# Kernel optimization log

Measured on AMD Instinct MI355X. Metric: run time of the kernel, lower is better.

## Reference

```python
import jax, jax.numpy as jnp
import numpy as np

H = 16
QK_NOPE = 128
QK_ROPE = 64
QK_HEAD = 192
V_HEAD = 128
KV_LORA = 512
Q_LORA = 1536
HIDDEN = 2048
ROPE_THETA = 500000.0
EPS = 1e-6


def _rms_norm(x, w, eps=EPS):
    var = jnp.mean(x * x, axis=-1, keepdims=True)
    return w * (x * jax.lax.rsqrt(var + eps))


def _rotate_half(x):
    d = x.shape[-1] // 2
    return jnp.concatenate([-x[..., d:], x[..., :d]], axis=-1)


def _rope_cos_sin(T, dim, theta, dtype):
    inv_freq = 1.0 / (theta ** (jnp.arange(0, dim, 2, dtype=jnp.float32) / dim))
    t = jnp.arange(T, dtype=jnp.float32)
    freqs = jnp.outer(t, inv_freq)               # [T, dim//2]
    emb = jnp.concatenate([freqs, freqs], axis=-1)  # [T, dim]
    return jnp.cos(emb).astype(dtype), jnp.sin(emb).astype(dtype)


def _apply_rope_interleave(q, k, cos, sin):
    # deinterleave: [x0,x1,x2,...] -> [x0,x2,... , x1,x3,...]
    def deint(x):
        return jnp.concatenate([x[..., 0::2], x[..., 1::2]], axis=-1)
    q, k = deint(q), deint(k)
    cos = cos[None, None]  # [1,1,T,d]
    sin = sin[None, None]
    q_e = q * cos + _rotate_half(q) * sin
    k_e = k * cos + _rotate_half(k) * sin
    return q_e, k_e


def setup_inputs() -> dict:
    key = jax.random.key(0)
    ks = jax.random.split(key, 8)
    s = 0.02
    B, T = 2, 2048
    return {
        "x": jax.random.normal(ks[0], (B, T, HIDDEN), jnp.float32),
        "q_a_w": jax.random.normal(ks[1], (HIDDEN, Q_LORA), jnp.float32) * s,
        "q_a_ln_w": jnp.ones((Q_LORA,), jnp.float32),
        "q_b_w": jax.random.normal(ks[2], (Q_LORA, H * QK_HEAD), jnp.float32) * s,
        "kv_a_w": jax.random.normal(ks[3], (HIDDEN, KV_LORA + QK_ROPE), jnp.float32) * s,
        "kv_a_ln_w": jnp.ones((KV_LORA,), jnp.float32),
        "kv_b_w": jax.random.normal(ks[4], (KV_LORA, H * (QK_NOPE + V_HEAD)), jnp.float32) * s,
        "o_w": jax.random.normal(ks[5], (H * V_HEAD, HIDDEN), jnp.float32) * s,
    }


def reference(x, q_a_w, q_a_ln_w, q_b_w, kv_a_w, kv_a_ln_w, kv_b_w, o_w):
    B, T, _ = x.shape
    scale = QK_HEAD ** -0.5

    # Q path: hidden -> q_lora -> RMSNorm -> H*qk_head
    q = _rms_norm(x @ q_a_w, q_a_ln_w) @ q_b_w
    q = q.reshape(B, T, H, QK_HEAD).transpose(0, 2, 1, 3)  # [B,H,T,qk_head]
    q_nope, q_rope = q[..., :QK_NOPE], q[..., QK_NOPE:]

    # KV path: hidden -> kv_lora + rope_dim
    ckv = x @ kv_a_w
    kv_c, k_rope = ckv[..., :KV_LORA], ckv[..., KV_LORA:]
    kv = _rms_norm(kv_c, kv_a_ln_w) @ kv_b_w
    kv = kv.reshape(B, T, H, QK_NOPE + V_HEAD).transpose(0, 2, 1, 3)
    k_nope, v = kv[..., :QK_NOPE], kv[..., QK_NOPE:]

    k_rope = k_rope.reshape(B, 1, T, QK_ROPE)
    cos, sin = _rope_cos_sin(T, QK_ROPE, ROPE_THETA, x.dtype)
    q_rope, k_rope = _apply_rope_interleave(q_rope, k_rope, cos, sin)
    k_rope = jnp.broadcast_to(k_rope, (B, H, T, QK_ROPE))

    qf = jnp.concatenate([q_nope, q_rope], axis=-1)  # [B,H,T,192]
    kf = jnp.concatenate([k_nope, k_rope], axis=-1)

    # causal SDPA
    scores = jnp.einsum("bhqd,bhkd->bhqk", qf, kf) * scale
    causal = jnp.tril(jnp.ones((T, T), bool))
    scores = jnp.where(causal[None, None], scores, jnp.finfo(scores.dtype).min)
    attn = jax.nn.softmax(scores, axis=-1)
    out = jnp.einsum("bhqk,bhkd->bhqd", attn, v)  # [B,H,T,128]
    out = out.transpose(0, 2, 1, 3).reshape(B, T, H * V_HEAD)
    return out @ o_w
```

## Files before the change

### kernel.cpp

```cpp
#include <hip/hip_runtime.h>
#include <hip/hip_bf16.h>
#include <cstdint>


typedef __bf16 bf16;
typedef __bf16 bf16x8 __attribute__((ext_vector_type(8)));
typedef __bf16 bf16x4v __attribute__((ext_vector_type(4)));
typedef float f32x4 __attribute__((ext_vector_type(4)));

#define TSEQ 2048
#define MR 4096

typedef const uint32_t __attribute__((address_space(1))) * gas1_t;
typedef uint32_t __attribute__((address_space(3))) * las3_t;

static __device__ __forceinline__ void gload_lds16(const void* g, void* l) {
  __builtin_amdgcn_global_load_lds(
      reinterpret_cast<gas1_t>(reinterpret_cast<uintptr_t>(g)),
      reinterpret_cast<las3_t>(reinterpret_cast<uintptr_t>(l)), 16, 0, 0);
}

static __device__ __forceinline__ f32x4 mfma16(bf16x8 a, bf16x8 b, f32x4 c) {
  return __builtin_amdgcn_mfma_f32_16x16x32_bf16(a, b, c, 0, 0, 0);
}


__global__ __launch_bounds__(256) void k_cvt_bf16(const float* __restrict__ in,
                                                  bf16* __restrict__ out) {
  int i = blockIdx.x * 256 + threadIdx.x;
  float4 f = reinterpret_cast<const float4*>(in)[i];
  bf16x4v o = {(bf16)f.x, (bf16)f.y, (bf16)f.z, (bf16)f.w};
  reinterpret_cast<bf16x4v*>(out)[i] = o;
}

__global__ __launch_bounds__(256) void k_zerofill(bf16* __restrict__ p) {
  uint4 z = make_uint4(0, 0, 0, 0);
  reinterpret_cast<uint4*>(p)[blockIdx.x * 256 + threadIdx.x] = z;
}

__global__ __launch_bounds__(256) void k_transpose(const float* __restrict__ W,
                                                   bf16* __restrict__ Wt,
                                                   int K, int N) {
  __shared__ float t[32][33];
  int bi = blockIdx.x, bj = blockIdx.y;
  int c = threadIdx.x & 31, r0 = threadIdx.x >> 5;
#pragma unroll
  for (int rr = 0; rr < 32; rr += 8)
    t[rr + r0][c] = W[(size_t)(bj * 32 + rr + r0) * N + bi * 32 + c];
  __syncthreads();
#pragma unroll
  for (int rr = 0; rr < 32; rr += 8)
    Wt[(size_t)(bi * 32 + rr + r0) * K + bj * 32 + c] = (bf16)t[c][rr + r0];
}

__global__ __launch_bounds__(64) void k_rope_table(float* __restrict__ rt) {
  int t = blockIdx.x * 2 + (threadIdx.x >> 5);
  int j = threadIdx.x & 31;
  float freq = exp2f(-(float)j * (1.0f / 32.0f) * log2f(500000.0f));
  float ang = (float)t * freq;
  rt[t * 64 + 2 * j] = cosf(ang);
  rt[t * 64 + 2 * j + 1] = sinf(ang);
}

template <int NCH>
__global__ __launch_bounds__(64) void k_rmsnorm(const bf16* __restrict__ in,
                                                const float* __restrict__ w,
                                                bf16* __restrict__ out,
                                                int in_stride) {
  int row = blockIdx.x, lane = threadIdx.x;
  const int D = NCH * 512;
  const bf16* ip = in + (size_t)row * in_stride;
  bf16x8 v[NCH];
  float ss = 0.f;
#pragma unroll
  for (int c = 0; c < NCH; ++c) {
    v[c] = *reinterpret_cast<const bf16x8*>(ip + c * 512 + lane * 8);
#pragma unroll
    for (int e = 0; e < 8; ++e) { float f = (float)v[c][e]; ss += f * f; }
  }
#pragma unroll
  for (int m = 1; m <= 32; m <<= 1) ss += __shfl_xor(ss, m);
  float rs = rsqrtf(ss / (float)D + 1e-6f);
  bf16* op = out + (size_t)row * D;
#pragma unroll
  for (int c = 0; c < NCH; ++c) {
    bf16x8 o;
#pragma unroll
    for (int e = 0; e < 8; ++e)
      o[e] = (bf16)((float)v[c][e] * rs * w[c * 512 + lane * 8 + e]);
    *reinterpret_cast<bf16x8*>(op + c * 512 + lane * 8) = o;
  }
}

__global__ __launch_bounds__(64) void k_kv_norm_rope(
    const bf16* __restrict__ in, const float* __restrict__ w,
    const float* __restrict__ rt, bf16* __restrict__ kvn,
    bf16* __restrict__ kr, int in_stride) {
  int row = blockIdx.x, lane = threadIdx.x;
  const bf16* ip = in + (size_t)row * in_stride;
  bf16x8 v = *reinterpret_cast<const bf16x8*>(ip + lane * 8);
  float ss = 0.f;
#pragma unroll
  for (int e = 0; e < 8; ++e) { float f = (float)v[e]; ss += f * f; }
#pragma unroll
  for (int m = 1; m <= 32; m <<= 1) ss += __shfl_xor(ss, m);
  float rs = rsqrtf(ss / 512.0f + 1e-6f);
  bf16x8 o;
#pragma unroll
  for (int e = 0; e < 8; ++e) o[e] = (bf16)((float)v[e] * rs * w[lane * 8 + e]);
  *reinterpret_cast<bf16x8*>(kvn + (size_t)row * 512 + lane * 8) = o;
  if (lane < 32) {
    int t = row & (TSEQ - 1);
    float x0 = (float)ip[512 + 2 * lane], x1 = (float)ip[512 + 2 * lane + 1];
    float c = rt[t * 64 + 2 * lane], s = rt[t * 64 + 2 * lane + 1];
    kr[(size_t)row * 64 + lane] = (bf16)(x0 * c - x1 * s);
    kr[(size_t)row * 64 + 32 + lane] = (bf16)(x1 * c + x0 * s);
  }
}

__global__ __launch_bounds__(256) void k_rope_q(const bf16* __restrict__ q,
                                                const float* __restrict__ rt,
                                                bf16* __restrict__ qr) {
  int idx = blockIdx.x * 256 + threadIdx.x;
  int j = idx & 31, h = (idx >> 5) & 15, row = idx >> 9;
  int t = row & (TSEQ - 1);
  const bf16* src = q + (size_t)row * 3072 + h * 192 + 128;
  float x0 = (float)src[2 * j], x1 = (float)src[2 * j + 1];
  float c = rt[t * 64 + 2 * j], s = rt[t * 64 + 2 * j + 1];
  bf16* dst = qr + ((size_t)row * 16 + h) * 64;
  dst[j] = (bf16)(x0 * c - x1 * s);
  dst[32 + j] = (bf16)(x1 * c + x0 * s);
}

#define GPH(BUF, MH, KH, DO_READB, STAGE_STMT, WAIT_STMT)                     \
  {                                                                           \
    if (DO_READB) {                                                           \
      _Pragma("unroll") for (int ni = 0; ni < 4; ++ni) {                      \
        int row = wn * 64 + ni * 16 + lr;                                     \
        breg[KH][ni] = *reinterpret_cast<const bf16x8*>(                      \
            &Bs[BUF][row * 64 + ((((KH)*4 + lg) ^ (row & 7)) * 8)]);          \
      }                                                                       \
    }                                                                         \
    bf16x8 af[4];                                                             \
    _Pragma("unroll") for (int mi = 0; mi < 4; ++mi) {                        \
      int row = wm * 128 + (MH)*64 + mi * 16 + lr;                            \
      af[mi] = *reinterpret_cast<const bf16x8*>(                              \
          &As[BUF][row * 64 + ((((KH)*4 + lg) ^ (row & 7)) * 8)]);            \
    }                                                                         \
    STAGE_STMT;                                                               \
    __builtin_amdgcn_s_barrier();                                             \
    __builtin_amdgcn_s_setprio(1);                                            \
    _Pragma("unroll") for (int mi = 0; mi < 4; ++mi)                          \
        _Pragma("unroll") for (int ni = 0; ni < 4; ++ni)                      \
            acc[(MH)*4 + mi][ni] =                                            \
        mfma16(af[mi], breg[KH][ni], acc[(MH)*4 + mi][ni]);                   \
    __builtin_amdgcn_s_setprio(0);                                            \
    WAIT_STMT;                                                                \
    __builtin_amdgcn_s_barrier();                                             \
  }

template <bool OUT_F32>
__global__ __launch_bounds__(512, 2) void k_gemm8(const bf16* __restrict__ A,
                                                  const bf16* __restrict__ Bt,
                                                  void* __restrict__ C, int M,
                                                  int N, int K) {
  __shared__ bf16 As[2][256 * 64];
  __shared__ bf16 Bs[2][256 * 64];
  const int tid = threadIdx.x, lane = tid & 63, w = tid >> 6;
  const int lg = lane >> 4, lr = lane & 15;
  const int wm = w >> 2, wn = w & 3;
  const int m0 = blockIdx.y * 256, n0 = blockIdx.x * 256;
  const int T = K >> 7;

  f32x4 acc[8][4] = {};
  bf16x8 breg[2][4];

  auto stageA = [&](int tau, int h) {
    char* dst = (char*)&As[tau & 1][0] + h * 16384;
#pragma unroll
    for (int j = 0; j < 2; ++j) {
      int c = j * 512 + tid;
      int row = c >> 3, slot = c & 7;
      gload_lds16(A + (size_t)(m0 + h * 128 + row) * K + tau * 64 +
                      ((slot ^ (row & 7)) * 8),
                  dst + (size_t)(j * 512 + w * 64) * 16);
    }
  };
  auto stageB = [&](int tau, int h) {
    char* dst = (char*)&Bs[tau & 1][0] + h * 16384;
#pragma unroll
    for (int j = 0; j < 2; ++j) {
      int c = j * 512 + tid;
      int row = c >> 3, slot = c & 7;
      gload_lds16(Bt + (size_t)(n0 + h * 128 + row) * K + tau * 64 +
                      ((slot ^ (row & 7)) * 8),
                  dst + (size_t)(j * 512 + w * 64) * 16);
    }
  };

  stageB(0, 0); stageB(0, 1); stageA(0, 0); stageA(0, 1);
  stageB(1, 0); stageB(1, 1); stageA(1, 0);
  asm volatile("s_waitcnt vmcnt(6)" ::: "memory");
  __builtin_amdgcn_s_barrier();

  for (int t = 0; t < T - 1; ++t) {
    const int s2 = 2 * t + 2, s3 = 2 * t + 3, a1 = 2 * t + 1;
    GPH(0, 0, 0, true,  stageA(a1, 1), ((void)0));
    GPH(0, 0, 1, true,  stageB(s2, 0), ((void)0));
    GPH(0, 1, 0, false, stageB(s2, 1), ((void)0));
    GPH(0, 1, 1, false, stageA(s2, 0),
        asm volatile("s_waitcnt vmcnt(6)" ::: "memory"));
    GPH(1, 0, 0, true,  stageA(s2, 1), ((void)0));
    GPH(1, 0, 1, true,  stageB(s3, 0), ((void)0));
    GPH(1, 1, 0, false, stageB(s3, 1), ((void)0));
    GPH(1, 1, 1, false, stageA(s3, 0),
        asm volatile("s_waitcnt vmcnt(6)" ::: "memory"));
  }
  {
    const int a1 = 2 * T - 1;
    GPH(0, 0, 0, true,  stageA(a1, 1), ((void)0));
    GPH(0, 0, 1, true,  ((void)0),     ((void)0));
    GPH(0, 1, 0, false, ((void)0),     ((void)0));
    GPH(0, 1, 1, false, ((void)0),
        asm volatile("s_waitcnt vmcnt(0)" ::: "memory"));
    GPH(1, 0, 0, true,  ((void)0), ((void)0));
    GPH(1, 0, 1, true,  ((void)0), ((void)0));
    GPH(1, 1, 0, false, ((void)0), ((void)0));
    GPH(1, 1, 1, false, ((void)0), ((void)0));
  }

#pragma unroll
  for (int mi = 0; mi < 8; ++mi)
#pragma unroll
    for (int ni = 0; ni < 4; ++ni) {
      int col = n0 + wn * 64 + ni * 16 + lr;
#pragma unroll
      for (int r = 0; r < 4; ++r) {
        int rowg = m0 + wm * 128 + mi * 16 + lg * 4 + r;
        if (OUT_F32)
          reinterpret_cast<float*>(C)[(size_t)rowg * N + col] = acc[mi][ni][r];
        else
          reinterpret_cast<bf16*>(C)[(size_t)rowg * N + col] =
              (bf16)acc[mi][ni][r];
      }
    }
}

__global__ __launch_bounds__(512, 2) void k_attn(const bf16* __restrict__ q,
                                                 const bf16* __restrict__ qr,
                                                 const bf16* __restrict__ kv,
                                                 const bf16* __restrict__ kr,
                                                 bf16* __restrict__ o) {
  __shared__ bf16 Kn[2][64 * 128];
  __shared__ bf16 Kr[2][64 * 64];
  __shared__ bf16 Vs[2][64 * 128];
  __shared__ bf16 Ps[8 * 1024];
  const int tid = threadIdx.x, lane = tid & 63, w = tid >> 6;
  const int lg = lane >> 4, lr = lane & 15;
  const float qsc = 0.07216878364870323f * 1.44269504088896f;
  uint4 vreg[2];
  const int vrr = tid & 31, vvc = tid >> 5;

  for (int t = 0; t < 2; ++t) {
    const int id = t ? 511 - (int)blockIdx.x : (int)blockIdx.x;
    const int qt = 15 - (id >> 5);
    const int bh = id & 31;
    const int b = bh >> 4, h = bh & 15;
    const int q0 = qt * 128;
    const size_t rowbase = (size_t)b * TSEQ;
    const int nkt = 2 * qt + 2;
    const int qg = q0 + w * 16 + lr;

    auto issue_loads = [&](int kbase, int buf) {
#pragma unroll
      for (int kk = 0; kk < 2; ++kk)
        vreg[kk] = *reinterpret_cast<const uint4*>(
            kv + (rowbase + kbase + vrr * 2 + kk) * 4096 + h * 256 + 128 +
            vvc * 8);
#pragma unroll
      for (int i = 0; i < 2; ++i) {
        int c = i * 512 + tid;
        int row = c >> 4, j = c & 15;
        gload_lds16(
            kv + (rowbase + kbase + row) * 4096 + h * 256 +
                ((j ^ (row & 15)) * 8),
            (char*)&Kn[buf][0] + (size_t)(i * 512 + w * 64) * 16);
      }
      {
        int row = tid >> 3, j = tid & 7;
        gload_lds16(kr + (rowbase + kbase + row) * 64 + ((j ^ (row & 7)) * 8),
                    (char*)&Kr[buf][0] + (size_t)(w * 64) * 16);
      }
    };

    auto write_vs = [&](int buf) {
      const int kb0 = vrr * 2;
      const int cC = kb0 >> 5, g = (kb0 >> 3) & 3, j0 = kb0 & 7;
      const uint32_t* r0 = reinterpret_cast<const uint32_t*>(&vreg[0]);
      const uint32_t* r1 = reinterpret_cast<const uint32_t*>(&vreg[1]);
#pragma unroll
      for (int e = 0; e < 8; ++e) {
        uint32_t h0 = (r0[e >> 1] >> ((e & 1) * 16)) & 0xffffu;
        uint32_t h1 = (r1[e >> 1] >> ((e & 1) * 16)) & 0xffffu;
        int vd = vvc * 8 + e;
        int slot = (vd & 15) ^ g;
        *reinterpret_cast<uint32_t*>(
            &Vs[buf][((cC * 8 + (vd >> 4)) * 4 + g) * 128 + slot * 8 + j0]) =
            h0 | (h1 << 16);
      }
    };

    bf16x8 qf[6];
    {
      const bf16* qp = q + (rowbase + qg) * 3072 + h * 192;
#pragma unroll
      for (int dc = 0; dc < 4; ++dc) {
        bf16x8 v = *reinterpret_cast<const bf16x8*>(qp + dc * 32 + lg * 8);
#pragma unroll
        for (int e = 0; e < 8; ++e) v[e] = (bf16)((float)v[e] * qsc);
        qf[dc] = v;
      }
      const bf16* qrp = qr + ((rowbase + qg) * 16 + h) * 64;
#pragma unroll
      for (int dc = 0; dc < 2; ++dc) {
        bf16x8 v = *reinterpret_cast<const bf16x8*>(qrp + dc * 32 + lg * 8);
#pragma unroll
        for (int e = 0; e < 8; ++e) v[e] = (bf16)((float)v[e] * qsc);
        qf[4 + dc] = v;
      }
    }

    f32x4 oacc[8] = {};
    float m_run = -1e30f, l_run = 0.f;

    issue_loads(0, 0);
    write_vs(0);
    __syncthreads();

    for (int kt = 0; kt < nkt; ++kt) {
      const int kbase = kt * 64;
      const int buf = kt & 1;
      const bool more = (kt + 1 < nkt);
      if (more) issue_loads(kbase + 64, buf ^ 1);

      if (kbase <= q0 + w * 16 + 15) {
        f32x4 sacc[4];
#pragma unroll
        for (int kb = 0; kb < 4; ++kb) {
          const int row = kb * 16 + lr;
          bf16x8 kf[6];
#pragma unroll
          for (int dc = 0; dc < 4; ++dc)
            kf[dc] = *reinterpret_cast<const bf16x8*>(
                &Kn[buf][row * 128 + (((dc * 4 + lg) ^ (row & 15)) * 8)]);
#pragma unroll
          for (int dc = 0; dc < 2; ++dc)
            kf[4 + dc] = *reinterpret_cast<const bf16x8*>(
                &Kr[buf][row * 64 + (((dc * 4 + lg) ^ (row & 7)) * 8)]);
          __builtin_amdgcn_s_setprio(1);
          f32x4 sa = {0.f, 0.f, 0.f, 0.f};
#pragma unroll
          for (int dc = 0; dc < 6; ++dc) sa = mfma16(kf[dc], qf[dc], sa);
          sacc[kb] = sa;
          __builtin_amdgcn_s_setprio(0);
        }
        float sv[4][4];
        if (kbase + 63 <= q0 + w * 16) {
#pragma unroll
          for (int kb = 0; kb < 4; ++kb)
#pragma unroll
            for (int r = 0; r < 4; ++r) sv[kb][r] = sacc[kb][r];
        } else {
#pragma unroll
          for (int kb = 0; kb < 4; ++kb)
#pragma unroll
            for (int r = 0; r < 4; ++r) {
              int kgl = kbase + kb * 16 + lg * 4 + r;
              sv[kb][r] = (kgl <= qg) ? sacc[kb][r] : -1e30f;
            }
        }
        float pmax = -1e30f;
#pragma unroll
        for (int kb = 0; kb < 4; ++kb)
#pragma unroll
          for (int r = 0; r < 4; ++r) pmax = fmaxf(pmax, sv[kb][r]);
        pmax = fmaxf(pmax, __shfl_xor(pmax, 16));
        pmax = fmaxf(pmax, __shfl_xor(pmax, 32));
        if (!__all(pmax - m_run <= 8.0f)) {
          float mnew = fmaxf(m_run, pmax);
          float alpha = exp2f(m_run - mnew);
          l_run *= alpha;
#pragma unroll
          for (int vb = 0; vb < 8; ++vb) {
            oacc[vb][0] *= alpha; oacc[vb][1] *= alpha;
            oacc[vb][2] *= alpha; oacc[vb][3] *= alpha;
          }
          m_run = mnew;
        }
        float ls = 0.f;
#pragma unroll
        for (int kb = 0; kb < 4; ++kb) {
          bf16x4v pw;
#pragma unroll
          for (int r = 0; r < 4; ++r) {
            float p = exp2f(sv[kb][r] - m_run);
            ls += p;
            pw[r] = (bf16)p;
          }
          *reinterpret_cast<bf16x4v*>(
              &Ps[w * 1024 + lr * 64 +
                  (((kb * 2 + (lg >> 1)) ^ (lr & 7)) * 8) + (lg & 1) * 4]) = pw;
        }
        ls += __shfl_xor(ls, 16);
        ls += __shfl_xor(ls, 32);
        l_run += ls;
#pragma unroll
        for (int c = 0; c < 2; ++c) {
          bf16x8 pb = *reinterpret_cast<const bf16x8*>(
              &Ps[w * 1024 + lr * 64 + (((c * 4 + lg) ^ (lr & 7)) * 8)]);
          __builtin_amdgcn_s_setprio(1);
#pragma unroll
          for (int vb = 0; vb < 8; ++vb) {
            bf16x8 av = *reinterpret_cast<const bf16x8*>(
                &Vs[buf][((c * 8 + vb) * 4 + lg) * 128 + (lr ^ lg) * 8]);
            oacc[vb] = mfma16(av, pb, oacc[vb]);
          }
          __builtin_amdgcn_s_setprio(0);
        }
      }
      if (more) write_vs(buf ^ 1);
      __syncthreads();
    }

    bf16* Os = &Kn[0][0] + w * 2048;
    {
      float inv = 1.0f / l_run;
#pragma unroll
      for (int vb = 0; vb < 8; ++vb) {
        bf16x4v ov;
#pragma unroll
        for (int r = 0; r < 4; ++r) ov[r] = (bf16)(oacc[vb][r] * inv);
        int slot16 = vb * 2 + (lg >> 1);
        *reinterpret_cast<bf16x4v*>(
            &Os[lr * 128 + ((slot16 ^ (lr & 7)) * 8) + (lg & 1) * 4]) = ov;
      }
    }
    asm volatile("s_waitcnt lgkmcnt(0)");
    __builtin_amdgcn_sched_barrier(0);
#pragma unroll
    for (int i = 0; i < 4; ++i) {
      const int r = i * 4 + lg;
      bf16x8 ov = *reinterpret_cast<const bf16x8*>(
          &Os[r * 128 + ((lr ^ (r & 7)) * 8)]);
      *reinterpret_cast<bf16x8*>(
          o + (rowbase + q0 + w * 16 + r) * 2048 + h * 128 + lr * 8) = ov;
    }
    __syncthreads();
  }
}

extern "C" void kernel_launch(void* const* d_in, const int* in_sizes, int n_in,
                              void* d_out, int out_size, void* d_ws,
                              size_t ws_size, hipStream_t stream) {
  (void)in_sizes; (void)n_in; (void)out_size; (void)ws_size;
  const float* x       = (const float*)d_in[0];
  const float* q_a_w   = (const float*)d_in[1];
  const float* q_a_ln  = (const float*)d_in[2];
  const float* q_b_w   = (const float*)d_in[3];
  const float* kv_a_w  = (const float*)d_in[4];
  const float* kv_a_ln = (const float*)d_in[5];
  const float* kv_b_w  = (const float*)d_in[6];
  const float* o_w     = (const float*)d_in[7];

  char* ws = (char*)d_ws;
  size_t off = 0;
  auto alloc = [&](size_t bytes) {
    void* p = ws + off;
    off += (bytes + 255) & ~(size_t)255;
    return p;
  };
  bf16* x_bf   = (bf16*)alloc((size_t)MR * 2048 * 2);
  bf16* ab_wt  = (bf16*)alloc((size_t)2304 * 2048 * 2);
  bf16* qb_wt  = (bf16*)alloc((size_t)3072 * 1536 * 2);
  bf16* kvb_wt = (bf16*)alloc((size_t)4096 * 512 * 2);
  bf16* o_wt   = (bf16*)alloc((size_t)2048 * 2048 * 2);
  float* rt    = (float*)alloc((size_t)2048 * 64 * 4);
  bf16* qac    = (bf16*)alloc((size_t)MR * 2304 * 2);
  bf16* q_a_n  = (bf16*)alloc((size_t)MR * 1536 * 2);
  bf16* kv_c_n = (bf16*)alloc((size_t)MR * 512 * 2);
  bf16* kr     = (bf16*)alloc((size_t)MR * 64 * 2);
  bf16* qbuf   = (bf16*)alloc((size_t)MR * 3072 * 2);
  bf16* qr     = (bf16*)alloc((size_t)MR * 16 * 64 * 2);
  bf16* kvbuf  = (bf16*)alloc((size_t)MR * 4096 * 2);
  bf16* attn_o = (bf16*)alloc((size_t)MR * 2048 * 2);

  k_cvt_bf16<<<8192, 256, 0, stream>>>(x, x_bf);
  k_transpose<<<dim3(1536 / 32, 2048 / 32), 256, 0, stream>>>(q_a_w, ab_wt, 2048, 1536);
  k_transpose<<<dim3(576 / 32, 2048 / 32), 256, 0, stream>>>(
      kv_a_w, ab_wt + (size_t)1536 * 2048, 2048, 576);
  k_zerofill<<<192, 256, 0, stream>>>(ab_wt + (size_t)2112 * 2048);
  k_transpose<<<dim3(3072 / 32, 1536 / 32), 256, 0, stream>>>(q_b_w, qb_wt, 1536, 3072);
  k_transpose<<<dim3(4096 / 32, 512 / 32), 256, 0, stream>>>(kv_b_w, kvb_wt, 512, 4096);
  k_transpose<<<dim3(2048 / 32, 2048 / 32), 256, 0, stream>>>(o_w, o_wt, 2048, 2048);
  k_rope_table<<<1024, 64, 0, stream>>>(rt);

  k_gemm8<false><<<dim3(9, 16), 512, 0, stream>>>(x_bf, ab_wt, qac, MR, 2304, 2048);
  k_rmsnorm<3><<<MR, 64, 0, stream>>>(qac, q_a_ln, q_a_n, 2304);
  k_kv_norm_rope<<<MR, 64, 0, stream>>>(qac + 1536, kv_a_ln, rt, kv_c_n, kr, 2304);
  k_gemm8<false><<<dim3(12, 16), 512, 0, stream>>>(q_a_n, qb_wt, qbuf, MR, 3072, 1536);
  k_rope_q<<<8192, 256, 0, stream>>>(qbuf, rt, qr);
  k_gemm8<false><<<dim3(16, 16), 512, 0, stream>>>(kv_c_n, kvb_wt, kvbuf, MR, 4096, 512);
  k_attn<<<dim3(256), 512, 0, stream>>>(qbuf, qr, kvbuf, kr, attn_o);
  k_gemm8<true><<<dim3(8, 16), 512, 0, stream>>>(attn_o, o_wt, d_out, MR, 2048, 2048);
}
```

Baseline: 301.2 us.

## Switch attention to 32x32x16 MFMA with split-K across wave pairs

The attention kernel now uses 32x32x16 bf16 MFMA tiles instead of 16x16x32. Each 32-query group is shared by two waves that each process half of every 64-key tile. The partial softmax states (m, l, O) of the two waves are merged through LDS at the end. The LDS layouts for K, V and P are redone to match, aiming for fewer LDS reads per MFMA and better matrix-core use. The cost is an extra merge step with three barriers, plus higher accumulator register pressure.

```diff
diff --git a/kernel.cpp b/kernel.cpp
--- a/kernel.cpp
+++ b/kernel.cpp
@@ -7,6 +7,7 @@
 typedef __bf16 bf16x8 __attribute__((ext_vector_type(8)));
 typedef __bf16 bf16x4v __attribute__((ext_vector_type(4)));
 typedef float f32x4 __attribute__((ext_vector_type(4)));
+typedef float f32x16 __attribute__((ext_vector_type(16)));
 
 #define TSEQ 2048
 #define MR 4096
@@ -22,6 +23,9 @@
 
 static __device__ __forceinline__ f32x4 mfma16(bf16x8 a, bf16x8 b, f32x4 c) {
   return __builtin_amdgcn_mfma_f32_16x16x32_bf16(a, b, c, 0, 0, 0);
+}
+static __device__ __forceinline__ f32x16 mfma32(bf16x8 a, bf16x8 b, f32x16 c) {
+  return __builtin_amdgcn_mfma_f32_32x32x16_bf16(a, b, c, 0, 0, 0);
 }
 
 
@@ -251,15 +255,22 @@
                                                  const bf16* __restrict__ kv,
                                                  const bf16* __restrict__ kr,
                                                  bf16* __restrict__ o) {
-  __shared__ bf16 Kn[2][64 * 128];
-  __shared__ bf16 Kr[2][64 * 64];
-  __shared__ bf16 Vs[2][64 * 128];
-  __shared__ bf16 Ps[8 * 1024];
+  __shared__ char arena[108544];
+  char* KnB = arena;
+  char* KrB = arena + 32768;
+  char* VsB = arena + 49152;
+  char* PsB = arena + 81920;
+  float* Mw = (float*)(arena + 106496);
+  float* Lw = (float*)(arena + 107520);
+
   const int tid = threadIdx.x, lane = tid & 63, w = tid >> 6;
-  const int lg = lane >> 4, lr = lane & 15;
+  const int hi = lane >> 5;
+  const int qidx = lane & 31;
+  const int g = w & 3, hh = w >> 2;
   const float qsc = 0.07216878364870323f * 1.44269504088896f;
   uint4 vreg[2];
   const int vrr = tid & 31, vvc = tid >> 5;
+  char* PsW = PsB + w * 3072;
 
   for (int t = 0; t < 2; ++t) {
     const int id = t ? 511 - (int)blockIdx.x : (int)blockIdx.x;
@@ -269,7 +280,8 @@
     const int q0 = qt * 128;
     const size_t rowbase = (size_t)b * TSEQ;
     const int nkt = 2 * qt + 2;
-    const int qg = q0 + w * 16 + lr;
+    const int qg = q0 + g * 32 + qidx;
+    const int krow = hh * 32 + qidx;
 
     auto issue_loads = [&](int kbase, int buf) {
 #pragma unroll
@@ -284,53 +296,55 @@
         gload_lds16(
             kv + (rowbase + kbase + row) * 4096 + h * 256 +
                 ((j ^ (row & 15)) * 8),
-            (char*)&Kn[buf][0] + (size_t)(i * 512 + w * 64) * 16);
+            KnB + buf * 16384 + (size_t)(i * 512 + w * 64) * 16);
       }
       {
         int row = tid >> 3, j = tid & 7;
         gload_lds16(kr + (rowbase + kbase + row) * 64 + ((j ^ (row & 7)) * 8),
-                    (char*)&Kr[buf][0] + (size_t)(w * 64) * 16);
+                    KrB + buf * 8192 + (size_t)(w * 64) * 16);
       }
     };
 
     auto write_vs = [&](int buf) {
-      const int kb0 = vrr * 2;
-      const int cC = kb0 >> 5, g = (kb0 >> 3) & 3, j0 = kb0 & 7;
       const uint32_t* r0 = reinterpret_cast<const uint32_t*>(&vreg[0]);
       const uint32_t* r1 = reinterpret_cast<const uint32_t*>(&vreg[1]);
+      const int s = vrr >> 2, sub = (vrr & 3) << 2;
 #pragma unroll
       for (int e = 0; e < 8; ++e) {
         uint32_t h0 = (r0[e >> 1] >> ((e & 1) * 16)) & 0xffffu;
         uint32_t h1 = (r1[e >> 1] >> ((e & 1) * 16)) & 0xffffu;
         int vd = vvc * 8 + e;
-        int slot = (vd & 15) ^ g;
         *reinterpret_cast<uint32_t*>(
-            &Vs[buf][((cC * 8 + (vd >> 4)) * 4 + g) * 128 + slot * 8 + j0]) =
+            VsB + buf * 16384 + vd * 128 + (((s ^ (vd & 7)) << 4) | sub)) =
             h0 | (h1 << 16);
       }
     };
 
-    bf16x8 qf[6];
+    bf16x8 qf[12];
     {
       const bf16* qp = q + (rowbase + qg) * 3072 + h * 192;
 #pragma unroll
-      for (int dc = 0; dc < 4; ++dc) {
-        bf16x8 v = *reinterpret_cast<const bf16x8*>(qp + dc * 32 + lg * 8);
+      for (int dc = 0; dc < 8; ++dc) {
+        bf16x8 v = *reinterpret_cast<const bf16x8*>(qp + dc * 16 + hi * 8);
 #pragma unroll
         for (int e = 0; e < 8; ++e) v[e] = (bf16)((float)v[e] * qsc);
         qf[dc] = v;
       }
       const bf16* qrp = qr + ((rowbase + qg) * 16 + h) * 64;
 #pragma unroll
-      for (int dc = 0; dc < 2; ++dc) {
-        bf16x8 v = *reinterpret_cast<const bf16x8*>(qrp + dc * 32 + lg * 8);
+      for (int dc = 0; dc < 4; ++dc) {
+        bf16x8 v = *reinterpret_cast<const bf16x8*>(qrp + dc * 16 + hi * 8);
 #pragma unroll
         for (int e = 0; e < 8; ++e) v[e] = (bf16)((float)v[e] * qsc);
-        qf[4 + dc] = v;
-      }
-    }
-
-    f32x4 oacc[8] = {};
+        qf[8 + dc] = v;
+      }
+    }
+
+    f32x16 oacc[4];
+#pragma unroll
+    for (int vb = 0; vb < 4; ++vb)
+#pragma unroll
+      for (int e = 0; e < 16; ++e) oacc[vb][e] = 0.f;
     float m_run = -1e30f, l_run = 0.f;
 
     issue_loads(0, 0);
@@ -343,87 +357,79 @@
       const bool more = (kt + 1 < nkt);
       if (more) issue_loads(kbase + 64, buf ^ 1);
 
-      if (kbase <= q0 + w * 16 + 15) {
-        f32x4 sacc[4];
-#pragma unroll
-        for (int kb = 0; kb < 4; ++kb) {
-          const int row = kb * 16 + lr;
-          bf16x8 kf[6];
-#pragma unroll
-          for (int dc = 0; dc < 4; ++dc)
-            kf[dc] = *reinterpret_cast<const bf16x8*>(
-                &Kn[buf][row * 128 + (((dc * 4 + lg) ^ (row & 15)) * 8)]);
-#pragma unroll
-          for (int dc = 0; dc < 2; ++dc)
-            kf[4 + dc] = *reinterpret_cast<const bf16x8*>(
-                &Kr[buf][row * 64 + (((dc * 4 + lg) ^ (row & 7)) * 8)]);
-          __builtin_amdgcn_s_setprio(1);
-          f32x4 sa = {0.f, 0.f, 0.f, 0.f};
-#pragma unroll
-          for (int dc = 0; dc < 6; ++dc) sa = mfma16(kf[dc], qf[dc], sa);
-          sacc[kb] = sa;
-          __builtin_amdgcn_s_setprio(0);
-        }
-        float sv[4][4];
-        if (kbase + 63 <= q0 + w * 16) {
-#pragma unroll
-          for (int kb = 0; kb < 4; ++kb)
-#pragma unroll
-            for (int r = 0; r < 4; ++r) sv[kb][r] = sacc[kb][r];
-        } else {
-#pragma unroll
-          for (int kb = 0; kb < 4; ++kb)
-#pragma unroll
-            for (int r = 0; r < 4; ++r) {
-              int kgl = kbase + kb * 16 + lg * 4 + r;
-              sv[kb][r] = (kgl <= qg) ? sacc[kb][r] : -1e30f;
-            }
-        }
+      if (kbase + hh * 32 <= q0 + g * 32 + 31) {
+        f32x16 sacc;
+#pragma unroll
+        for (int e = 0; e < 16; ++e) sacc[e] = 0.f;
+        __builtin_amdgcn_s_setprio(1);
+#pragma unroll
+        for (int dc = 0; dc < 8; ++dc) {
+          bf16x8 kf = *reinterpret_cast<const bf16x8*>(
+              KnB + buf * 16384 + krow * 256 +
+              ((((dc << 1) | hi) ^ (krow & 15)) << 4));
+          sacc = mfma32(kf, qf[dc], sacc);
+        }
+#pragma unroll
+        for (int dc = 0; dc < 4; ++dc) {
+          bf16x8 kf = *reinterpret_cast<const bf16x8*>(
+              KrB + buf * 8192 + krow * 128 +
+              ((((dc << 1) | hi) ^ (krow & 7)) << 4));
+          sacc = mfma32(kf, qf[8 + dc], sacc);
+        }
+        __builtin_amdgcn_s_setprio(0);
+        const bool open = (kbase + hh * 32 + 31 <= q0 + g * 32);
+        float sv[16];
         float pmax = -1e30f;
 #pragma unroll
-        for (int kb = 0; kb < 4; ++kb)
-#pragma unroll
-          for (int r = 0; r < 4; ++r) pmax = fmaxf(pmax, sv[kb][r]);
-        pmax = fmaxf(pmax, __shfl_xor(pmax, 16));
+        for (int rg = 0; rg < 16; ++rg) {
+          float val = sacc[rg];
+          if (!open) {
+            int kgl = kbase + hh * 32 + (rg & 3) + ((rg >> 2) << 3) + (hi << 2);
+            val = (kgl <= qg) ? val : -1e30f;
+          }
+          sv[rg] = val;
+          pmax = fmaxf(pmax, val);
+        }
         pmax = fmaxf(pmax, __shfl_xor(pmax, 32));
         if (!__all(pmax - m_run <= 8.0f)) {
           float mnew = fmaxf(m_run, pmax);
           float alpha = exp2f(m_run - mnew);
           l_run *= alpha;
 #pragma unroll
-          for (int vb = 0; vb < 8; ++vb) {
-            oacc[vb][0] *= alpha; oacc[vb][1] *= alpha;
-            oacc[vb][2] *= alpha; oacc[vb][3] *= alpha;
-          }
+          for (int vb = 0; vb < 4; ++vb)
+#pragma unroll
+            for (int e = 0; e < 16; ++e) oacc[vb][e] *= alpha;
           m_run = mnew;
         }
         float ls = 0.f;
 #pragma unroll
-        for (int kb = 0; kb < 4; ++kb) {
+        for (int qd = 0; qd < 4; ++qd) {
           bf16x4v pw;
 #pragma unroll
           for (int r = 0; r < 4; ++r) {
-            float p = exp2f(sv[kb][r] - m_run);
+            float p = exp2f(sv[qd * 4 + r] - m_run);
             ls += p;
             pw[r] = (bf16)p;
           }
           *reinterpret_cast<bf16x4v*>(
-              &Ps[w * 1024 + lr * 64 +
-                  (((kb * 2 + (lg >> 1)) ^ (lr & 7)) * 8) + (lg & 1) * 4]) = pw;
-        }
-        ls += __shfl_xor(ls, 16);
+              PsW + qidx * 96 + (((qd ^ ((qidx >> 2) & 3)) << 4) | (hi << 3))) =
+              pw;
+        }
         ls += __shfl_xor(ls, 32);
         l_run += ls;
 #pragma unroll
-        for (int c = 0; c < 2; ++c) {
+        for (int cc = 0; cc < 2; ++cc) {
           bf16x8 pb = *reinterpret_cast<const bf16x8*>(
-              &Ps[w * 1024 + lr * 64 + (((c * 4 + lg) ^ (lr & 7)) * 8)]);
+              PsW + qidx * 96 +
+              ((((cc << 1) | hi) ^ ((qidx >> 2) & 3)) << 4));
           __builtin_amdgcn_s_setprio(1);
 #pragma unroll
-          for (int vb = 0; vb < 8; ++vb) {
+          for (int vb = 0; vb < 4; ++vb) {
+            int vd = vb * 32 + qidx;
             bf16x8 av = *reinterpret_cast<const bf16x8*>(
-                &Vs[buf][((c * 8 + vb) * 4 + lg) * 128 + (lr ^ lg) * 8]);
-            oacc[vb] = mfma16(av, pb, oacc[vb]);
+                VsB + buf * 16384 + vd * 128 +
+                ((((hh << 2) | (cc << 1) | hi) ^ (vd & 7)) << 4));
+            oacc[vb] = mfma32(av, pb, oacc[vb]);
           }
           __builtin_amdgcn_s_setprio(0);
         }
@@ -432,28 +438,67 @@
       __syncthreads();
     }
 
-    bf16* Os = &Kn[0][0] + w * 2048;
-    {
-      float inv = 1.0f / l_run;
-#pragma unroll
-      for (int vb = 0; vb < 8; ++vb) {
-        bf16x4v ov;
-#pragma unroll
-        for (int r = 0; r < 4; ++r) ov[r] = (bf16)(oacc[vb][r] * inv);
-        int slot16 = vb * 2 + (lg >> 1);
-        *reinterpret_cast<bf16x4v*>(
-            &Os[lr * 128 + ((slot16 ^ (lr & 7)) * 8) + (lg & 1) * 4]) = ov;
-      }
-    }
-    asm volatile("s_waitcnt lgkmcnt(0)");
-    __builtin_amdgcn_sched_barrier(0);
-#pragma unroll
-    for (int i = 0; i < 4; ++i) {
-      const int r = i * 4 + lg;
-      bf16x8 ov = *reinterpret_cast<const bf16x8*>(
-          &Os[r * 128 + ((lr ^ (r & 7)) * 8)]);
-      *reinterpret_cast<bf16x8*>(
-          o + (rowbase + q0 + w * 16 + r) * 2048 + h * 128 + lr * 8) = ov;
+    if (lane < 32) {
+      Mw[w * 32 + lane] = m_run;
+      Lw[w * 32 + lane] = l_run;
+    }
+    __syncthreads();
+    float m_o = Mw[(w ^ 4) * 32 + qidx], l_o = Lw[(w ^ 4) * 32 + qidx];
+    float mstar = fmaxf(m_run, m_o);
+    float a_s = exp2f(m_run - mstar);
+    float lstar = l_run * a_s + l_o * exp2f(m_o - mstar);
+    char* Ob = arena + g * 17408 + qidx * 544;
+    if (hh == 0) {
+#pragma unroll
+      for (int vb = 0; vb < 4; ++vb)
+#pragma unroll
+        for (int rq = 0; rq < 4; ++rq) {
+          f32x4 tv;
+#pragma unroll
+          for (int r = 0; r < 4; ++r) tv[r] = a_s * oacc[vb][rq * 4 + r];
+          int s16 = vb * 8 + rq * 2 + hi;
+          *reinterpret_cast<f32x4*>(
+              Ob + ((s16 ^ ((qidx >> 2) & 7)) << 4)) = tv;
+        }
+    }
+    __syncthreads();
+    bf16x4v ov[4][4];
+    if (hh == 1) {
+      float inv = 1.0f / lstar;
+#pragma unroll
+      for (int vb = 0; vb < 4; ++vb)
+#pragma unroll
+        for (int rq = 0; rq < 4; ++rq) {
+          int s16 = vb * 8 + rq * 2 + hi;
+          f32x4 tv = *reinterpret_cast<const f32x4*>(
+              Ob + ((s16 ^ ((qidx >> 2) & 7)) << 4));
+#pragma unroll
+          for (int r = 0; r < 4; ++r)
+            ov[vb][rq][r] =
+                (bf16)((tv[r] + a_s * oacc[vb][rq * 4 + r]) * inv);
+        }
+    }
+    __syncthreads();
+    if (hh == 1) {
+      char* OsG = arena + g * 8192;
+#pragma unroll
+      for (int vb = 0; vb < 4; ++vb)
+#pragma unroll
+        for (int rq = 0; rq < 4; ++rq)
+          *reinterpret_cast<bf16x4v*>(
+              OsG + qidx * 256 + ((((vb * 4 + rq) ^ (qidx & 7)) << 4) |
+                                  (hi << 3))) = ov[vb][rq];
+      asm volatile("s_waitcnt lgkmcnt(0)");
+      __builtin_amdgcn_sched_barrier(0);
+      const int lg2 = (lane >> 4) & 3, lr2 = lane & 15;
+#pragma unroll
+      for (int i = 0; i < 8; ++i) {
+        int r = i * 4 + lg2;
+        bf16x8 tv = *reinterpret_cast<const bf16x8*>(
+            OsG + r * 256 + ((lr2 ^ (r & 7)) << 4));
+        *reinterpret_cast<bf16x8*>(
+            o + (rowbase + q0 + g * 32 + r) * 2048 + h * 128 + lr2 * 8) = tv;
+      }
     }
     __syncthreads();
   }
```

Measured after the change: 319.2 us. 1.06x slower.

## Fuse preprocessing kernels into one launch and remap GEMM blocks across XCDs

Applied to the files above, without the earlier changes.

Merges the fp32-to-bf16 conversion, five weight transposes, zero-fill and rope-table kernels into a single k_prep launch that dispatches on block index, removing several launch gaps. The GEMM kernel also remaps its linear workgroup id so that consecutive tiles land on the same XCD (grouping by orig&7), intended to improve L2 reuse across the eight chiplets. This assumes the block count is divisible by 8 and adds branch overhead to the prep blocks.

```diff
diff --git a/kernel.cpp b/kernel.cpp
--- a/kernel.cpp
+++ b/kernel.cpp
@@ -24,25 +24,9 @@
   return __builtin_amdgcn_mfma_f32_16x16x32_bf16(a, b, c, 0, 0, 0);
 }
 
-
-__global__ __launch_bounds__(256) void k_cvt_bf16(const float* __restrict__ in,
-                                                  bf16* __restrict__ out) {
-  int i = blockIdx.x * 256 + threadIdx.x;
-  float4 f = reinterpret_cast<const float4*>(in)[i];
-  bf16x4v o = {(bf16)f.x, (bf16)f.y, (bf16)f.z, (bf16)f.w};
-  reinterpret_cast<bf16x4v*>(out)[i] = o;
-}
-
-__global__ __launch_bounds__(256) void k_zerofill(bf16* __restrict__ p) {
-  uint4 z = make_uint4(0, 0, 0, 0);
-  reinterpret_cast<uint4*>(p)[blockIdx.x * 256 + threadIdx.x] = z;
-}
-
-__global__ __launch_bounds__(256) void k_transpose(const float* __restrict__ W,
-                                                   bf16* __restrict__ Wt,
-                                                   int K, int N) {
-  __shared__ float t[32][33];
-  int bi = blockIdx.x, bj = blockIdx.y;
+static __device__ __forceinline__ void do_transpose(
+    const float* __restrict__ W, bf16* __restrict__ Wt, int K, int N, int bi,
+    int bj, float (*t)[33]) {
   int c = threadIdx.x & 31, r0 = threadIdx.x >> 5;
 #pragma unroll
   for (int rr = 0; rr < 32; rr += 8)
@@ -53,13 +37,53 @@
     Wt[(size_t)(bi * 32 + rr + r0) * K + bj * 32 + c] = (bf16)t[c][rr + r0];
 }
 
-__global__ __launch_bounds__(64) void k_rope_table(float* __restrict__ rt) {
-  int t = blockIdx.x * 2 + (threadIdx.x >> 5);
-  int j = threadIdx.x & 31;
-  float freq = exp2f(-(float)j * (1.0f / 32.0f) * log2f(500000.0f));
-  float ang = (float)t * freq;
-  rt[t * 64 + 2 * j] = cosf(ang);
-  rt[t * 64 + 2 * j + 1] = sinf(ang);
+#define PREP_BLOCKS (8192 + 3072 + 1152 + 4608 + 2048 + 4096 + 192 + 256)
+
+__global__ __launch_bounds__(256) void k_prep(
+    const float* __restrict__ x, const float* __restrict__ q_a_w,
+    const float* __restrict__ kv_a_w, const float* __restrict__ q_b_w,
+    const float* __restrict__ kv_b_w, const float* __restrict__ o_w,
+    bf16* __restrict__ x_bf, bf16* __restrict__ ab_wt,
+    bf16* __restrict__ qb_wt, bf16* __restrict__ kvb_wt,
+    bf16* __restrict__ o_wt, float* __restrict__ rt) {
+  __shared__ float t[32][33];
+  int nb = blockIdx.x;
+  const int tid = threadIdx.x;
+  if (nb < 8192) {
+    int i = nb * 256 + tid;
+    float4 f = reinterpret_cast<const float4*>(x)[i];
+    bf16x4v o = {(bf16)f.x, (bf16)f.y, (bf16)f.z, (bf16)f.w};
+    reinterpret_cast<bf16x4v*>(x_bf)[i] = o;
+    return;
+  }
+  nb -= 8192;
+  if (nb < 3072) { do_transpose(q_a_w, ab_wt, 2048, 1536, nb % 48, nb / 48, t); return; }
+  nb -= 3072;
+  if (nb < 1152) {
+    do_transpose(kv_a_w, ab_wt + (size_t)1536 * 2048, 2048, 576, nb % 18, nb / 18, t);
+    return;
+  }
+  nb -= 1152;
+  if (nb < 4608) { do_transpose(q_b_w, qb_wt, 1536, 3072, nb % 96, nb / 96, t); return; }
+  nb -= 4608;
+  if (nb < 2048) { do_transpose(kv_b_w, kvb_wt, 512, 4096, nb % 128, nb / 128, t); return; }
+  nb -= 2048;
+  if (nb < 4096) { do_transpose(o_w, o_wt, 2048, 2048, nb % 64, nb / 64, t); return; }
+  nb -= 4096;
+  if (nb < 192) {
+    uint4 z = make_uint4(0, 0, 0, 0);
+    reinterpret_cast<uint4*>(ab_wt + (size_t)2112 * 2048)[nb * 256 + tid] = z;
+    return;
+  }
+  nb -= 192;
+  {
+    int idx = nb * 256 + tid;
+    int tt = idx >> 5, j = idx & 31;
+    float freq = exp2f(-(float)j * (1.0f / 32.0f) * log2f(500000.0f));
+    float ang = (float)tt * freq;
+    rt[tt * 64 + 2 * j] = cosf(ang);
+    rt[tt * 64 + 2 * j + 1] = sinf(ang);
+  }
 }
 
 template <int NCH>
@@ -169,7 +193,11 @@
   const int tid = threadIdx.x, lane = tid & 63, w = tid >> 6;
   const int lg = lane >> 4, lr = lane & 15;
   const int wm = w >> 2, wn = w & 3;
-  const int m0 = blockIdx.y * 256, n0 = blockIdx.x * 256;
+  const int nwg = gridDim.x * gridDim.y;
+  const int orig = blockIdx.y * gridDim.x + blockIdx.x;
+  const int cpx = nwg >> 3;
+  const int wgid = (orig & 7) * cpx + (orig >> 3);
+  const int m0 = (wgid / gridDim.x) * 256, n0 = (wgid % gridDim.x) * 256;
   const int T = K >> 7;
 
   f32x4 acc[8][4] = {};
@@ -494,16 +522,9 @@
   bf16* kvbuf  = (bf16*)alloc((size_t)MR * 4096 * 2);
   bf16* attn_o = (bf16*)alloc((size_t)MR * 2048 * 2);
 
-  k_cvt_bf16<<<8192, 256, 0, stream>>>(x, x_bf);
-  k_transpose<<<dim3(1536 / 32, 2048 / 32), 256, 0, stream>>>(q_a_w, ab_wt, 2048, 1536);
-  k_transpose<<<dim3(576 / 32, 2048 / 32), 256, 0, stream>>>(
-      kv_a_w, ab_wt + (size_t)1536 * 2048, 2048, 576);
-  k_zerofill<<<192, 256, 0, stream>>>(ab_wt + (size_t)2112 * 2048);
-  k_transpose<<<dim3(3072 / 32, 1536 / 32), 256, 0, stream>>>(q_b_w, qb_wt, 1536, 3072);
-  k_transpose<<<dim3(4096 / 32, 512 / 32), 256, 0, stream>>>(kv_b_w, kvb_wt, 512, 4096);
-  k_transpose<<<dim3(2048 / 32, 2048 / 32), 256, 0, stream>>>(o_w, o_wt, 2048, 2048);
-  k_rope_table<<<1024, 64, 0, stream>>>(rt);
-
+  k_prep<<<PREP_BLOCKS, 256, 0, stream>>>(x, q_a_w, kv_a_w, q_b_w, kv_b_w,
+                                          o_w, x_bf, ab_wt, qb_wt, kvb_wt,
+                                          o_wt, rt);
   k_gemm8<false><<<dim3(9, 16), 512, 0, stream>>>(x_bf, ab_wt, qac, MR, 2304, 2048);
   k_rmsnorm<3><<<MR, 64, 0, stream>>>(qac, q_a_ln, q_a_n, 2304);
   k_kv_norm_rope<<<MR, 64, 0, stream>>>(qac + 1536, kv_a_ln, rt, kv_c_n, kr, 2304);
```

New measurement: 287.2 us. -4.6%, faster.
